# Kernel optimization log

Hardware: AMD Instinct MI355X
Metric: run time of the kernel (lower is better)

Reference implementation:

```python
import jax, jax.numpy as jnp
import numpy as np

ALPHA = 0.2  # LeakyReLU negative slope
NEG = -9e15


def gat_layer(h, adj, W, a):
    # Faithful to the torch GAT: e_ij = leakyrelu(a^T [Wh_i || Wh_j])
    # = leakyrelu(a_src . Wh_i + a_dst . Wh_j); avoids the NxNx2F materialization.
    Wh = h @ W                              # [N, F]
    Fo = W.shape[1]
    a_src, a_dst = a[:Fo, 0], a[Fo:, 0]
    e = jax.nn.leaky_relu(
        (Wh @ a_src)[:, None] + (Wh @ a_dst)[None, :], negative_slope=ALPHA
    )                                        # [N, N]
    e = jnp.where(adj > 0, e, NEG)
    att = jax.nn.softmax(e, axis=1)          # dropout p=0 (eval)
    return jax.nn.elu(att @ Wh)


def gru_cell(x, h, W_ih, W_hh, b_ih, b_hh):
    # PyTorch GRUCell semantics.
    gi = x @ W_ih.T + b_ih                   # [N, 3F]
    gh = h @ W_hh.T + b_hh
    i_r, i_z, i_n = jnp.split(gi, 3, axis=1)
    h_r, h_z, h_n = jnp.split(gh, 3, axis=1)
    r = jax.nn.sigmoid(i_r + h_r)
    z = jax.nn.sigmoid(i_z + h_z)
    n = jnp.tanh(i_n + r * h_n)
    return (1.0 - z) * n + z * h


def setup_inputs() -> dict:
    key = jax.random.key(0)
    ks = jax.random.split(key, 10)
    N, nfeat, nhid, nout = 8192, 256, 128, 128
    x = jax.random.normal(ks[0], (N, nfeat), dtype=jnp.float32)
    # sparse random binary adjacency (~32 avg degree) + self loops
    adj = (jax.random.uniform(ks[1], (N, N)) < 0.004).astype(jnp.float32)
    adj = jnp.maximum(adj, jnp.eye(N, dtype=jnp.float32))
    h_prev = jnp.zeros((N, nout), dtype=jnp.float32)

    def xavier(k, shape, gain=1.414):
        fan_in, fan_out = shape[0], shape[1]
        b = gain * np.sqrt(6.0 / (fan_in + fan_out))
        return jax.random.uniform(k, shape, jnp.float32, -b, b)

    W1 = xavier(ks[2], (nfeat, nhid))
    a1 = xavier(ks[3], (2 * nhid, 1))
    W2 = xavier(ks[4], (nhid, nout))
    a2 = xavier(ks[5], (2 * nout, 1))
    s = 1.0 / np.sqrt(nout)
    W_ih = jax.random.uniform(ks[6], (3 * nout, nout), jnp.float32, -s, s)
    W_hh = jax.random.uniform(ks[7], (3 * nout, nout), jnp.float32, -s, s)
    b_ih = jax.random.uniform(ks[8], (3 * nout,), jnp.float32, -s, s)
    b_hh = jax.random.uniform(ks[9], (3 * nout,), jnp.float32, -s, s)
    return {"x": x, "adj": adj, "h_prev": h_prev, "W1": W1, "a1": a1,
            "W2": W2, "a2": a2, "W_ih": W_ih, "W_hh": W_hh,
            "b_ih": b_ih, "b_hh": b_hh}


def reference(x, adj, h_prev, W1, a1, W2, a2, W_ih, W_hh, b_ih, b_hh):
    x1 = gat_layer(x, adj, W1, a1)
    h_spat = gat_layer(x1, adj, W2, a2)
    return gru_cell(h_spat, h_prev, W_ih, W_hh, b_ih, b_hh)
```

## Files before the change

kernel.cpp:

```cpp
#include <hip/hip_runtime.h>
#include <math.h>

#define N_NODES 8192
#define CAP 128
#define LRELU_ALPHA 0.2f

typedef float v4f __attribute__((ext_vector_type(4)));

template <int K, int ROWS>
__device__ __forceinline__ void gemm_from_lds(
    int r0, int t, const float* As, const float* __restrict__ W,
    const float* __restrict__ a, float* __restrict__ Wh, float* __restrict__ src,
    float* __restrict__ dst, float (*red)[4][2]) {
  constexpr int RH = ROWS / 2;
  int c = t & 127, half = t >> 7;
  float acc[RH];
#pragma unroll
  for (int r = 0; r < RH; r++) acc[r] = 0.f;
  const float* Asl = As + (half * RH) * K;
#pragma unroll 8
  for (int k = 0; k < K; k++) {
    float wv = W[k * 128 + c];
#pragma unroll
    for (int r = 0; r < RH; r++) acc[r] += Asl[r * K + k] * wv;
  }
  float as = a[c], ad = a[128 + c];
  int wv_id = t >> 6, lane = t & 63;
#pragma unroll
  for (int r = 0; r < RH; r++) {
    int row = half * RH + r;
    Wh[(size_t)(r0 + row) * 128 + c] = acc[r];
    float s = acc[r] * as, d = acc[r] * ad;
#pragma unroll
    for (int off = 32; off; off >>= 1) {
      s += __shfl_xor(s, off);
      d += __shfl_xor(d, off);
    }
    if (lane == 0) { red[wv_id][r][0] = s; red[wv_id][r][1] = d; }
  }
  __syncthreads();
  if (t < ROWS) {
    int h = t / RH, rr = t - h * RH, wa = h * 2;
    src[r0 + t] = red[wa][rr][0] + red[wa + 1][rr][0];
    dst[r0 + t] = red[wa][rr][1] + red[wa + 1][rr][1];
  }
}

__device__ __forceinline__ void agg_pair(
    int i0, int s, int t, const float* __restrict__ Wh, const float* __restrict__ src,
    const float* __restrict__ dst, const int* __restrict__ idxbuf,
    const int* __restrict__ counts, float* tile, int (*jn)[128], float (*w)[128],
    float (*redm)[2], float (*reds)[2], float (*accs)[4][128]) {
  int half = t >> 7;
  int u = t & 127;
  int wv = (t >> 6) & 1;
  int i = i0 + s * 2 + half;
  int c = counts[i];
  float si = src[i];
  float e = -1e30f;
  if (u < c) {
    int j = idxbuf[(size_t)i * CAP + u];
    jn[half][u] = j;
    float xv = si + dst[j];
    e = xv > 0.f ? xv : LRELU_ALPHA * xv;
  }
  float m = e;
#pragma unroll
  for (int off = 32; off; off >>= 1) m = fmaxf(m, __shfl_xor(m, off));
  if ((t & 63) == 0) redm[half][wv] = m;
  __syncthreads();
  float M = fmaxf(redm[half][0], redm[half][1]);
  float ex = 0.f;
  if (u < c) {
    ex = expf(e - M);
    w[half][u] = ex;
  }
  float ss = ex;
#pragma unroll
  for (int off = 32; off; off >>= 1) ss += __shfl_xor(ss, off);
  if ((t & 63) == 0) reds[half][wv] = ss;
  __syncthreads();
  float inv = 1.f / (reds[half][0] + reds[half][1]);
  int slot = (t >> 5) & 3, col4 = t & 31;
  const float4* Wh4 = (const float4*)Wh;
  float ax = 0.f, ay = 0.f, az = 0.f, aw = 0.f;
  int k = slot;
  for (; k + 4 < c; k += 8) {
    float w0 = w[half][k], w1 = w[half][k + 4];
    float4 v0 = Wh4[(size_t)jn[half][k] * 32 + col4];
    float4 v1 = Wh4[(size_t)jn[half][k + 4] * 32 + col4];
    ax += w0 * v0.x + w1 * v1.x;
    ay += w0 * v0.y + w1 * v1.y;
    az += w0 * v0.z + w1 * v1.z;
    aw += w0 * v0.w + w1 * v1.w;
  }
  if (k < c) {
    float w0 = w[half][k];
    float4 v0 = Wh4[(size_t)jn[half][k] * 32 + col4];
    ax += w0 * v0.x; ay += w0 * v0.y; az += w0 * v0.z; aw += w0 * v0.w;
  }
  *(float4*)&accs[half][slot][col4 * 4] = make_float4(ax, ay, az, aw);
  __syncthreads();
  float r = accs[half][0][u] + accs[half][1][u] + accs[half][2][u] + accs[half][3][u];
  r *= inv;
  tile[(s * 2 + half) * 128 + u] = r > 0.f ? r : expf(r) - 1.f;
  __syncthreads();
}

__global__ __launch_bounds__(256) void kA(
    const float* __restrict__ adj, int* __restrict__ idxbuf, int* __restrict__ counts,
    const float* __restrict__ x, const float* __restrict__ W1, const float* __restrict__ a1,
    float* __restrict__ Wh1, float* __restrict__ src1, float* __restrict__ dst1,
    const float* __restrict__ Wi, const float* __restrict__ Whm, float* __restrict__ WiT,
    float* __restrict__ WhT) {
  __shared__ float As[8 * 256];
  __shared__ float red[4][4][2];
  __shared__ int jn[CAP];
  __shared__ int cnt;
  int t = threadIdx.x, b = blockIdx.x;
  if (b < N_NODES) {
    if (t == 0) cnt = 0;
    __syncthreads();
    const v4f* row = (const v4f*)(adj + (size_t)b * N_NODES);
    v4f v[8];
#pragma unroll
    for (int u = 0; u < 8; u++) v[u] = __builtin_nontemporal_load(row + t + 256 * u);
#pragma unroll
    for (int u = 0; u < 8; u++) {
      int n = (v[u].x > 0.f) + (v[u].y > 0.f) + (v[u].z > 0.f) + (v[u].w > 0.f);
      if (n) {
        int p = atomicAdd(&cnt, n);
        int j0 = (t + 256 * u) * 4;
        if (v[u].x > 0.f) { if (p < CAP) jn[p] = j0;     p++; }
        if (v[u].y > 0.f) { if (p < CAP) jn[p] = j0 + 1; p++; }
        if (v[u].z > 0.f) { if (p < CAP) jn[p] = j0 + 2; p++; }
        if (v[u].w > 0.f) { if (p < CAP) jn[p] = j0 + 3; p++; }
      }
    }
    __syncthreads();
    int c = cnt > CAP ? CAP : cnt;
    if (t < c) idxbuf[(size_t)b * CAP + t] = jn[t];
    if (t == 0) counts[b] = c;
  } else if (b < N_NODES + 1024) {
    int tile = b - N_NODES;
    const float4* Ab4 = (const float4*)(x + (size_t)tile * 8 * 256);
    float4* As4 = (float4*)As;
#pragma unroll
    for (int l = t; l < 8 * 256 / 4; l += 256) As4[l] = Ab4[l];
    __syncthreads();
    gemm_from_lds<256, 8>(tile * 8, t, As, W1, a1, Wh1, src1, dst1, red);
  } else {
    for (int n = (b - N_NODES - 1024) * 256 + t; n < 384 * 128; n += 64 * 256) {
      int r = n >> 7, c = n & 127;
      WiT[c * 384 + r] = Wi[n];
      WhT[c * 384 + r] = Whm[n];
    }
  }
}

__global__ __launch_bounds__(256, 8) void kB(
    const float* __restrict__ Wh1, const float* __restrict__ src1,
    const float* __restrict__ dst1, const int* __restrict__ idxbuf,
    const int* __restrict__ counts, const float* __restrict__ W2, const float* __restrict__ a2,
    float* __restrict__ Wh2, float* __restrict__ src2, float* __restrict__ dst2) {
  __shared__ float tile[4 * 128];
  __shared__ float red[4][4][2];
  __shared__ int jn[2][128];
  __shared__ float w[2][128];
  __shared__ float redm[2][2];
  __shared__ float reds[2][2];
  __shared__ float accs[2][4][128];
  int t = threadIdx.x, b = blockIdx.x;
  int i0 = b * 4;
#pragma unroll 1
  for (int s = 0; s < 2; s++)
    agg_pair(i0, s, t, Wh1, src1, dst1, idxbuf, counts, tile, jn, w, redm, reds, accs);
  gemm_from_lds<128, 4>(i0, t, tile, W2, a2, Wh2, src2, dst2, red);
}

__global__ __launch_bounds__(256, 8) void kC(
    const float* __restrict__ Wh2, const float* __restrict__ src2,
    const float* __restrict__ dst2, const int* __restrict__ idxbuf,
    const int* __restrict__ counts, const float* __restrict__ hprev,
    const float* __restrict__ WiT, const float* __restrict__ WhT,
    const float* __restrict__ b_ih, const float* __restrict__ b_hh, float* __restrict__ outp) {
  __shared__ float tile[4 * 128];
  __shared__ float hs[4 * 128];
  __shared__ int jn[2][128];
  __shared__ float w[2][128];
  __shared__ float redm[2][2];
  __shared__ float reds[2][2];
  __shared__ float accs[2][4][128];
  int t = threadIdx.x, b = blockIdx.x;
  int i0 = b * 4;
  if (t < 128) ((float4*)hs)[t] = ((const float4*)(hprev + (size_t)i0 * 128))[t];
#pragma unroll 1
  for (int s = 0; s < 2; s++)
    agg_pair(i0, s, t, Wh2, src2, dst2, idxbuf, counts, tile, jn, w, redm, reds, accs);
  int c = t & 127, half = t >> 7;
  const float* xsl = tile + half * 2 * 128;
  const float* hsl = hs + half * 2 * 128;
  float rg[2], zg[2];
  {
    float ai[2] = {0.f, 0.f}, ah[2] = {0.f, 0.f};
#pragma unroll 4
    for (int k = 0; k < 128; k++) {
      float wi = WiT[k * 384 + c], wh = WhT[k * 384 + c];
#pragma unroll
      for (int r = 0; r < 2; r++) { ai[r] += xsl[r * 128 + k] * wi; ah[r] += hsl[r * 128 + k] * wh; }
    }
    float bi = b_ih[c], bh = b_hh[c];
#pragma unroll
    for (int r = 0; r < 2; r++) rg[r] = 1.f / (1.f + expf(-(ai[r] + bi + ah[r] + bh)));
  }
  {
    float ai[2] = {0.f, 0.f}, ah[2] = {0.f, 0.f};
#pragma unroll 4
    for (int k = 0; k < 128; k++) {
      float wi = WiT[k * 384 + 128 + c], wh = WhT[k * 384 + 128 + c];
#pragma unroll
      for (int r = 0; r < 2; r++) { ai[r] += xsl[r * 128 + k] * wi; ah[r] += hsl[r * 128 + k] * wh; }
    }
    float bi = b_ih[128 + c], bh = b_hh[128 + c];
#pragma unroll
    for (int r = 0; r < 2; r++) zg[r] = 1.f / (1.f + expf(-(ai[r] + bi + ah[r] + bh)));
  }
  {
    float ai[2] = {0.f, 0.f}, ah[2] = {0.f, 0.f};
#pragma unroll 4
    for (int k = 0; k < 128; k++) {
      float wi = WiT[k * 384 + 256 + c], wh = WhT[k * 384 + 256 + c];
#pragma unroll
      for (int r = 0; r < 2; r++) { ai[r] += xsl[r * 128 + k] * wi; ah[r] += hsl[r * 128 + k] * wh; }
    }
    float bi = b_ih[256 + c], bh = b_hh[256 + c];
#pragma unroll
    for (int r = 0; r < 2; r++) {
      float n = tanhf(ai[r] + bi + rg[r] * (ah[r] + bh));
      outp[(size_t)(i0 + half * 2 + r) * 128 + c] =
          (1.f - zg[r]) * n + zg[r] * hsl[r * 128 + c];
    }
  }
}

extern "C" void kernel_launch(void* const* d_in, const int* in_sizes, int n_in,
                              void* d_out, int out_size, void* d_ws, size_t ws_size,
                              hipStream_t stream) {
  const float* x     = (const float*)d_in[0];
  const float* adj   = (const float*)d_in[1];
  const float* hprev = (const float*)d_in[2];
  const float* W1    = (const float*)d_in[3];
  const float* a1    = (const float*)d_in[4];
  const float* W2    = (const float*)d_in[5];
  const float* a2    = (const float*)d_in[6];
  const float* Wi    = (const float*)d_in[7];
  const float* Whm   = (const float*)d_in[8];
  const float* b_ih  = (const float*)d_in[9];
  const float* b_hh  = (const float*)d_in[10];
  float* outp = (float*)d_out;

  char* p = (char*)d_ws;
  float* Wh1    = (float*)p; p += (size_t)N_NODES * 128 * 4;
  float* Wh2    = (float*)p; p += (size_t)N_NODES * 128 * 4;
  float* src1   = (float*)p; p += (size_t)N_NODES * 4;
  float* dst1   = (float*)p; p += (size_t)N_NODES * 4;
  float* src2   = (float*)p; p += (size_t)N_NODES * 4;
  float* dst2   = (float*)p; p += (size_t)N_NODES * 4;
  float* WiT    = (float*)p; p += (size_t)384 * 128 * 4;
  float* WhT    = (float*)p; p += (size_t)384 * 128 * 4;
  int*   counts = (int*)p;   p += (size_t)N_NODES * 4;
  int*   idxbuf = (int*)p;   p += (size_t)N_NODES * CAP * 4;

  kA<<<N_NODES + 1024 + 64, 256, 0, stream>>>(adj, idxbuf, counts, x, W1, a1, Wh1, src1, dst1,
                                              Wi, Whm, WiT, WhT);
  kB<<<N_NODES / 4, 256, 0, stream>>>(Wh1, src1, dst1, idxbuf, counts, W2, a2, Wh2, src2, dst2);
  kC<<<N_NODES / 4, 256, 0, stream>>>(Wh2, src2, dst2, idxbuf, counts, hprev, WiT, WhT, b_ih,
                                      b_hh, outp);
}
```

Before: 458.0 us.

## Fuse adjacency compaction into layer-2 aggregation kernel, one node per block

```diff
diff --git a/kernel.cpp b/kernel.cpp
--- a/kernel.cpp
+++ b/kernel.cpp
@@ -43,6 +43,132 @@
     int h = t / RH, rr = t - h * RH, wa = h * 2;
     src[r0 + t] = red[wa][rr][0] + red[wa + 1][rr][0];
     dst[r0 + t] = red[wa][rr][1] + red[wa + 1][rr][1];
+  }
+}
+
+__global__ __launch_bounds__(256) void kA(
+    const float* __restrict__ x, const float* __restrict__ W1, const float* __restrict__ a1,
+    float* __restrict__ Wh1, float* __restrict__ src1, float* __restrict__ dst1,
+    const float* __restrict__ Wi, const float* __restrict__ Whm, float* __restrict__ WiT,
+    float* __restrict__ WhT) {
+  __shared__ float As[8 * 256];
+  __shared__ float red[4][4][2];
+  int t = threadIdx.x, b = blockIdx.x;
+  if (b < 1024) {
+    const float4* Ab4 = (const float4*)(x + (size_t)b * 8 * 256);
+    float4* As4 = (float4*)As;
+#pragma unroll
+    for (int l = t; l < 8 * 256 / 4; l += 256) As4[l] = Ab4[l];
+    __syncthreads();
+    gemm_from_lds<256, 8>(b * 8, t, As, W1, a1, Wh1, src1, dst1, red);
+  } else {
+    for (int n = (b - 1024) * 256 + t; n < 384 * 128; n += 64 * 256) {
+      int r = n >> 7, c = n & 127;
+      WiT[c * 384 + r] = Wi[n];
+      WhT[c * 384 + r] = Whm[n];
+    }
+  }
+}
+
+__global__ __launch_bounds__(256) void kB(
+    const float* __restrict__ adj, const float* __restrict__ Wh1,
+    const float* __restrict__ src1, const float* __restrict__ dst1, int* __restrict__ idxbuf,
+    int* __restrict__ counts, const float* __restrict__ W2, const float* __restrict__ a2,
+    float* __restrict__ Wh2, float* __restrict__ src2, float* __restrict__ dst2) {
+  __shared__ int jn[CAP];
+  __shared__ float w[CAP];
+  __shared__ float redm[4];
+  __shared__ float reds[4];
+  __shared__ float accs[8][128];
+  __shared__ float tile[128];
+  __shared__ float part[2][128];
+  __shared__ int cnt;
+  int i = blockIdx.x, t = threadIdx.x;
+  if (t == 0) cnt = 0;
+  __syncthreads();
+  const v4f* row = (const v4f*)(adj + (size_t)i * N_NODES);
+  v4f v[8];
+#pragma unroll
+  for (int u = 0; u < 8; u++) v[u] = __builtin_nontemporal_load(row + t + 256 * u);
+#pragma unroll
+  for (int u = 0; u < 8; u++) {
+    int n = (v[u].x > 0.f) + (v[u].y > 0.f) + (v[u].z > 0.f) + (v[u].w > 0.f);
+    if (n) {
+      int p = atomicAdd(&cnt, n);
+      int j0 = (t + 256 * u) * 4;
+      if (v[u].x > 0.f) { if (p < CAP) jn[p] = j0;     p++; }
+      if (v[u].y > 0.f) { if (p < CAP) jn[p] = j0 + 1; p++; }
+      if (v[u].z > 0.f) { if (p < CAP) jn[p] = j0 + 2; p++; }
+      if (v[u].w > 0.f) { if (p < CAP) jn[p] = j0 + 3; p++; }
+    }
+  }
+  __syncthreads();
+  int c = cnt > CAP ? CAP : cnt;
+  if (t < c) idxbuf[(size_t)i * CAP + t] = jn[t];
+  if (t == 0) counts[i] = c;
+  float si = src1[i];
+  float e = -1e30f;
+  if (t < c) {
+    float xv = si + dst1[jn[t]];
+    e = xv > 0.f ? xv : LRELU_ALPHA * xv;
+  }
+  float m = e;
+#pragma unroll
+  for (int off = 32; off; off >>= 1) m = fmaxf(m, __shfl_xor(m, off));
+  if ((t & 63) == 0) redm[t >> 6] = m;
+  __syncthreads();
+  float M = fmaxf(redm[0], redm[1]);
+  float ex = 0.f;
+  if (t < c) {
+    ex = expf(e - M);
+    w[t] = ex;
+  }
+  float ss = ex;
+#pragma unroll
+  for (int off = 32; off; off >>= 1) ss += __shfl_xor(ss, off);
+  if ((t & 63) == 0) reds[t >> 6] = ss;
+  __syncthreads();
+  float inv = 1.f / (reds[0] + reds[1]);
+  int slot = t >> 5, col4 = t & 31;
+  const float4* Wh4 = (const float4*)Wh1;
+  float ax = 0.f, ay = 0.f, az = 0.f, aw = 0.f;
+  for (int k = slot; k < c; k += 8) {
+    float w0 = w[k];
+    float4 v0 = Wh4[(size_t)jn[k] * 32 + col4];
+    ax += w0 * v0.x; ay += w0 * v0.y; az += w0 * v0.z; aw += w0 * v0.w;
+  }
+  *(float4*)&accs[slot][col4 * 4] = make_float4(ax, ay, az, aw);
+  __syncthreads();
+  if (t < 128) {
+    float r = 0.f;
+#pragma unroll
+    for (int s2 = 0; s2 < 8; s2++) r += accs[s2][t];
+    r *= inv;
+    tile[t] = r > 0.f ? r : expf(r) - 1.f;
+  }
+  __syncthreads();
+  int cc = t & 127, half = t >> 7;
+  float acc = 0.f;
+  int k0 = half * 64;
+#pragma unroll 8
+  for (int k = k0; k < k0 + 64; k++) acc += tile[k] * W2[k * 128 + cc];
+  part[half][cc] = acc;
+  __syncthreads();
+  if (t < 128) {
+    float wh = part[0][t] + part[1][t];
+    Wh2[(size_t)i * 128 + t] = wh;
+    float s = wh * a2[t], d = wh * a2[128 + t];
+#pragma unroll
+    for (int off = 32; off; off >>= 1) {
+      s += __shfl_xor(s, off);
+      d += __shfl_xor(d, off);
+    }
+    if ((t & 63) == 0) { redm[t >> 6] = s; reds[t >> 6] = d; }
+  }
+  __syncthreads();
+  if (t == 0) {
+    src2[i] = redm[0] + redm[1];
+    dst2[i] = reds[0] + reds[1];
   }
 }
 
@@ -105,77 +231,6 @@
   r *= inv;
   tile[(s * 2 + half) * 128 + u] = r > 0.f ? r : expf(r) - 1.f;
   __syncthreads();
-}
-
-__global__ __launch_bounds__(256) void kA(
-    const float* __restrict__ adj, int* __restrict__ idxbuf, int* __restrict__ counts,
-    const float* __restrict__ x, const float* __restrict__ W1, const float* __restrict__ a1,
-    float* __restrict__ Wh1, float* __restrict__ src1, float* __restrict__ dst1,
-    const float* __restrict__ Wi, const float* __restrict__ Whm, float* __restrict__ WiT,
-    float* __restrict__ WhT) {
-  __shared__ float As[8 * 256];
-  __shared__ float red[4][4][2];
-  __shared__ int jn[CAP];
-  __shared__ int cnt;
-  int t = threadIdx.x, b = blockIdx.x;
-  if (b < N_NODES) {
-    if (t == 0) cnt = 0;
-    __syncthreads();
-    const v4f* row = (const v4f*)(adj + (size_t)b * N_NODES);
-    v4f v[8];
-#pragma unroll
-    for (int u = 0; u < 8; u++) v[u] = __builtin_nontemporal_load(row + t + 256 * u);
-#pragma unroll
-    for (int u = 0; u < 8; u++) {
-      int n = (v[u].x > 0.f) + (v[u].y > 0.f) + (v[u].z > 0.f) + (v[u].w > 0.f);
-      if (n) {
-        int p = atomicAdd(&cnt, n);
-        int j0 = (t + 256 * u) * 4;
-        if (v[u].x > 0.f) { if (p < CAP) jn[p] = j0;     p++; }
-        if (v[u].y > 0.f) { if (p < CAP) jn[p] = j0 + 1; p++; }
-        if (v[u].z > 0.f) { if (p < CAP) jn[p] = j0 + 2; p++; }
-        if (v[u].w > 0.f) { if (p < CAP) jn[p] = j0 + 3; p++; }
-      }
-    }
-    __syncthreads();
-    int c = cnt > CAP ? CAP : cnt;
-    if (t < c) idxbuf[(size_t)b * CAP + t] = jn[t];
-    if (t == 0) counts[b] = c;
-  } else if (b < N_NODES + 1024) {
-    int tile = b - N_NODES;
-    const float4* Ab4 = (const float4*)(x + (size_t)tile * 8 * 256);
-    float4* As4 = (float4*)As;
-#pragma unroll
-    for (int l = t; l < 8 * 256 / 4; l += 256) As4[l] = Ab4[l];
-    __syncthreads();
-    gemm_from_lds<256, 8>(tile * 8, t, As, W1, a1, Wh1, src1, dst1, red);
-  } else {
-    for (int n = (b - N_NODES - 1024) * 256 + t; n < 384 * 128; n += 64 * 256) {
-      int r = n >> 7, c = n & 127;
-      WiT[c * 384 + r] = Wi[n];
-      WhT[c * 384 + r] = Whm[n];
-    }
-  }
-}
-
-__global__ __launch_bounds__(256, 8) void kB(
-    const float* __restrict__ Wh1, const float* __restrict__ src1,
-    const float* __restrict__ dst1, const int* __restrict__ idxbuf,
-    const int* __restrict__ counts, const float* __restrict__ W2, const float* __restrict__ a2,
-    float* __restrict__ Wh2, float* __restrict__ src2, float* __restrict__ dst2) {
-  __shared__ float tile[4 * 128];
-  __shared__ float red[4][4][2];
-  __shared__ int jn[2][128];
-  __shared__ float w[2][128];
-  __shared__ float redm[2][2];
-  __shared__ float reds[2][2];
-  __shared__ float accs[2][4][128];
-  int t = threadIdx.x, b = blockIdx.x;
-  int i0 = b * 4;
-#pragma unroll 1
-  for (int s = 0; s < 2; s++)
-    agg_pair(i0, s, t, Wh1, src1, dst1, idxbuf, counts, tile, jn, w, redm, reds, accs);
-  gemm_from_lds<128, 4>(i0, t, tile, W2, a2, Wh2, src2, dst2, red);
 }
 
 __global__ __launch_bounds__(256, 8) void kC(
@@ -271,9 +326,9 @@
   int*   counts = (int*)p;   p += (size_t)N_NODES * 4;
   int*   idxbuf = (int*)p;   p += (size_t)N_NODES * CAP * 4;
 
-  kA<<<N_NODES + 1024 + 64, 256, 0, stream>>>(adj, idxbuf, counts, x, W1, a1, Wh1, src1, dst1,
-                                              Wi, Whm, WiT, WhT);
-  kB<<<N_NODES / 4, 256, 0, stream>>>(Wh1, src1, dst1, idxbuf, counts, W2, a2, Wh2, src2, dst2);
+  kA<<<1024 + 64, 256, 0, stream>>>(x, W1, a1, Wh1, src1, dst1, Wi, Whm, WiT, WhT);
+  kB<<<N_NODES, 256, 0, stream>>>(adj, Wh1, src1, dst1, idxbuf, counts, W2, a2, Wh2, src2,
+                                  dst2);
   kC<<<N_NODES / 4, 256, 0, stream>>>(Wh2, src2, dst2, idxbuf, counts, hprev, WiT, WhT, b_ih,
                                       b_hh, outp);
 }
```

Result: no change. 466.6 us (+1.9%).
